# Optimization experiments

Measured on AMD Instinct MI355X. Metric: run time of the kernel, lower is better.

Reference implementation:

```python
import jax, jax.numpy as jnp
import numpy as np

POOL = 7
IMG = 1024.0
NUM_CLASSES = 2
R = 1000


def crop_and_resize(feat, boxes, pool):
    # feat: [C,H,W]; boxes: [N,4] normalized (y1,x1,y2,x2); returns [N,C,pool,pool]
    C, H, W = feat.shape
    y1, x1, y2, x2 = boxes[:, 0], boxes[:, 1], boxes[:, 2], boxes[:, 3]
    t = jnp.arange(pool, dtype=feat.dtype) / (pool - 1)
    ys = (y1[:, None] + (y2 - y1)[:, None] * t[None, :]) * (H - 1)  # [N,P]
    xs = (x1[:, None] + (x2 - x1)[:, None] * t[None, :]) * (W - 1)  # [N,P]
    vy = (ys >= 0) & (ys <= H - 1)
    vx = (xs >= 0) & (xs <= W - 1)
    yf = jnp.floor(ys)
    xf = jnp.floor(xs)
    wy = (ys - yf)[None, :, :, None]  # [1,N,P,1]
    wx = (xs - xf)[None, :, None, :]  # [1,N,1,P]
    y0 = jnp.clip(yf, 0, H - 1).astype(jnp.int32)
    y1i = jnp.clip(yf + 1, 0, H - 1).astype(jnp.int32)
    x0 = jnp.clip(xf, 0, W - 1).astype(jnp.int32)
    x1i = jnp.clip(xf + 1, 0, W - 1).astype(jnp.int32)

    def g(yi, xi):  # gather -> [C,N,P,P]
        return feat[:, yi[:, :, None], xi[:, None, :]]

    val = (g(y0, x0) * (1 - wy) * (1 - wx)
           + g(y0, x1i) * (1 - wy) * wx
           + g(y1i, x0) * wy * (1 - wx)
           + g(y1i, x1i) * wy * wx)
    mask = (vy[:, :, None] & vx[:, None, :])[None]  # extrapolation value 0
    return jnp.where(mask, val, 0.0).transpose(1, 0, 2, 3)


def roi_align(feats, rois_flat):
    # rois_flat: [N,4] in pixel coords (x1,y1,x2,y2)
    x1, y1, x2, y2 = rois_flat[:, 0], rois_flat[:, 1], rois_flat[:, 2], rois_flat[:, 3]
    lvl = jnp.log2(jnp.sqrt((y2 - y1) * (x2 - x1)) / 224.0)
    lvl = jnp.clip(jnp.round(lvl) + 4, 2, 5)
    boxes = rois_flat[:, jnp.array([1, 0, 3, 2])] / IMG  # (y1,x1,y2,x2) normalized
    crops = jnp.stack([crop_and_resize(f[0], boxes, POOL) for f in feats])  # [4,N,C,P,P]
    sel = (lvl[None, :] == jnp.arange(2, 6, dtype=lvl.dtype)[:, None])       # [4,N]
    return jnp.sum(jnp.where(sel[:, :, None, None, None], crops, 0.0), axis=0)  # [N,C,P,P]


def setup_inputs() -> dict:
    key = jax.random.key(0)
    ks = jax.random.split(key, 24)
    feat2 = jax.random.normal(ks[0], (1, 256, 256, 256), jnp.float32)
    feat3 = jax.random.normal(ks[1], (1, 256, 128, 128), jnp.float32)
    feat4 = jax.random.normal(ks[2], (1, 256, 64, 64), jnp.float32)
    feat5 = jax.random.normal(ks[3], (1, 256, 32, 32), jnp.float32)
    x1 = jax.random.uniform(ks[4], (1, R), minval=0.0, maxval=900.0)
    y1 = jax.random.uniform(ks[5], (1, R), minval=0.0, maxval=900.0)
    w = jax.random.uniform(ks[6], (1, R), minval=16.0, maxval=400.0)
    h = jax.random.uniform(ks[7], (1, R), minval=16.0, maxval=400.0)
    rois = jnp.stack([x1, y1, jnp.minimum(x1 + w, 1023.0), jnp.minimum(y1 + h, 1023.0)], axis=-1)
    s = 0.02
    params = dict(
        conv_w=s * jax.random.normal(ks[8], (1024, 256, POOL, POOL), jnp.float32),
        conv_b=jnp.zeros((1024,), jnp.float32),
        bn_gamma=jnp.ones((1024,), jnp.float32),
        bn_beta=jnp.zeros((1024,), jnp.float32),
        bn_mean=jnp.zeros((1024,), jnp.float32),
        bn_var=jnp.ones((1024,), jnp.float32),
        fc1_w=s * jax.random.normal(ks[9], (1024, 1024), jnp.float32),
        fc1_b=jnp.zeros((1024,), jnp.float32),
        fc2_w=s * jax.random.normal(ks[10], (1024, 1024), jnp.float32),
        fc2_b=jnp.zeros((1024,), jnp.float32),
        cls_w=s * jax.random.normal(ks[11], (NUM_CLASSES, 1024), jnp.float32),
        cls_b=jnp.zeros((NUM_CLASSES,), jnp.float32),
        bbox_w=s * jax.random.normal(ks[12], (NUM_CLASSES * 4, 1024), jnp.float32),
        bbox_b=jnp.zeros((NUM_CLASSES * 4,), jnp.float32),
    )
    return dict(feat2=feat2, feat3=feat3, feat4=feat4, feat5=feat5, rois=rois, **params)


def reference(feat2, feat3, feat4, feat5, rois, conv_w, conv_b, bn_gamma, bn_beta,
              bn_mean, bn_var, fc1_w, fc1_b, fc2_w, fc2_b, cls_w, cls_b, bbox_w, bbox_b):
    roi_number = rois.shape[1]
    pooled = roi_align([feat2, feat3, feat4, feat5], rois.reshape(-1, 4))  # [N,256,7,7]
    # conv1 (7x7 valid on 7x7 input -> 1x1 spatial) + BN (inference stats, eps=1e-3)
    y = jnp.einsum('nchw,ochw->no', pooled, conv_w) + conv_b
    y = (y - bn_mean) / jnp.sqrt(bn_var + 1e-3) * bn_gamma + bn_beta
    h = jax.nn.relu(y @ fc1_w.T + fc1_b)
    h = jax.nn.relu(h @ fc2_w.T + fc2_b)
    logits = h @ cls_w.T + cls_b
    probs = jax.nn.softmax(logits, axis=-1)
    bbox = h @ bbox_w.T + bbox_b
    return (logits.reshape(1, roi_number, NUM_CLASSES),
            probs.reshape(1, roi_number, NUM_CLASSES),
            bbox.reshape(1, roi_number, NUM_CLASSES, 4))
```

## Files before the change

### kernel.cpp

```cpp
#include <hip/hip_runtime.h>
#include <cstdint>
#include <cstddef>

typedef __attribute__((ext_vector_type(8))) short bf16x8;
typedef __attribute__((ext_vector_type(4))) float f32x4;

#define POOLK 12544

#define TOFF2 0
#define TOFF3 16777216
#define TOFF4 20971520
#define TOFF5 22020096

__device__ __forceinline__ void gld16(const void* g, void* l) {
    __builtin_amdgcn_global_load_lds(
        (const __attribute__((address_space(1))) void*)g,
        (__attribute__((address_space(3))) void*)l, 16, 0, 0);
}
__device__ __forceinline__ unsigned short f32_to_bf16(float f) {
    union { float f; unsigned u; } x; x.f = f;
    return (unsigned short)((x.u + 0x7FFFu + ((x.u >> 16) & 1u)) >> 16);
}
__device__ __forceinline__ float bf16_to_f32(unsigned short s) {
    return __uint_as_float(((unsigned)s) << 16);
}

__global__ __launch_bounds__(256) void feat_tr_kernel(
    const float* __restrict__ f2, const float* __restrict__ f3,
    const float* __restrict__ f4, const float* __restrict__ f5,
    unsigned short* __restrict__ T)
{
    __shared__ __align__(16) unsigned short sh[128 * 256];
    int b = blockIdx.x;
    const float* src; unsigned short* dst; int P;
    if (b < 512)      { src = f2; dst = T + TOFF2; P = 65536; }
    else if (b < 640) { src = f3; dst = T + TOFF3; P = 16384; b -= 512; }
    else if (b < 672) { src = f4; dst = T + TOFF4; P = 4096;  b -= 640; }
    else              { src = f5; dst = T + TOFF5; P = 1024;  b -= 672; }
    const int p0 = b * 128;
    const int t = threadIdx.x;
    const int lane5 = t & 31;
    const int x4 = lane5 * 4;
    const int fx = (lane5 & 7) << 3;

#pragma unroll
    for (int it = 0; it < 8; ++it) {
        float4 v[4];
        int cs[4];
#pragma unroll
        for (int u = 0; u < 4; ++u) {
            cs[u] = it * 32 + u * 8 + (t >> 5);
            v[u] = *(const float4*)(src + (size_t)cs[u] * P + p0 + x4);
        }
#pragma unroll
        for (int u = 0; u < 4; ++u) {
            const int cp = cs[u] ^ fx;
            float vv[4] = {v[u].x, v[u].y, v[u].z, v[u].w};
#pragma unroll
            for (int i = 0; i < 4; ++i)
                sh[(x4 + i) * 256 + cp] = f32_to_bf16(vv[i]);
        }
    }
    __syncthreads();

    const int c0 = lane5 * 8;
#pragma unroll
    for (int oz = 0; oz < 16; ++oz) {
        const int pp = oz * 8 + (t >> 5);
        const int cr = c0 ^ (((pp >> 2) & 7) << 3);
        const bf16x8 vv = *(const bf16x8*)&sh[pp * 256 + cr];
        *(bf16x8*)(dst + (size_t)(p0 + pp) * 256 + c0) = vv;
    }
}

__global__ __launch_bounds__(256) void gather_prep_kernel(
    const unsigned short* __restrict__ T, const float* __restrict__ rois,
    unsigned short* __restrict__ pooled, int nroi,
    const float* __restrict__ conv_w, unsigned short* __restrict__ convw_bf,
    const float* __restrict__ fc1_w, unsigned short* __restrict__ fc1w_bf,
    const float* __restrict__ fc2_w, unsigned short* __restrict__ fc2w_bf)
{
    const int t = threadIdx.x;
    int b = blockIdx.x;

    if (b >= 2048) {
        b -= 2048;
        if (b < 1024) {
            __shared__ __align__(16) unsigned short shw[POOLK];
            const float* srow = conv_w + (size_t)b * POOLK;
            for (int k4 = t; k4 < 3136; k4 += 256) {
                const float4 v = *(const float4*)(srow + k4 * 4);
                ushort4 o4;
                o4.x = f32_to_bf16(v.x); o4.y = f32_to_bf16(v.y);
                o4.z = f32_to_bf16(v.z); o4.w = f32_to_bf16(v.w);
                *(ushort4*)(&shw[k4 * 4]) = o4;
            }
            __syncthreads();
            unsigned short* drow = convw_bf + (size_t)b * POOLK;
            for (int e = t; e < 1568; e += 256) {
                const int p = e * 8;
                const int ij = p >> 8, c0 = p & 255;
                bf16x8 o8;
#pragma unroll
                for (int c = 0; c < 8; ++c) o8[c] = (short)shw[(c0 + c) * 49 + ij];
                *(bf16x8*)(drow + p) = o8;
            }
        } else {
            b -= 1024;
            const float* src = (b < 256) ? fc1_w : fc2_w;
            unsigned short* dst = (b < 256) ? fc1w_bf : fc2w_bf;
            const int base = (b & 255) * 4096 + t * 16;
#pragma unroll
            for (int u = 0; u < 4; ++u) {
                const float4 v = *(const float4*)(src + base + u * 4);
                ushort4 o4;
                o4.x = f32_to_bf16(v.x); o4.y = f32_to_bf16(v.y);
                o4.z = f32_to_bf16(v.z); o4.w = f32_to_bf16(v.w);
                *(ushort4*)(dst + base + u * 4) = o4;
            }
        }
        return;
    }

    const int n = b >> 1;
    const int half = b & 1;
    unsigned short* orow = pooled + (size_t)n * POOLK;
    if (n >= nroi) {
        const bf16x8 z = {};
        const int base = half * 6272;
        for (int k = base + t * 8; k < base + 6272; k += 2048) *(bf16x8*)(orow + k) = z;
        return;
    }
    __shared__ int sy0[7], sy1[7], sx0[7], sx1[7];
    __shared__ float swy[7], swx[7], svy[7], svx[7];

    const float rx1 = rois[n*4+0], ry1 = rois[n*4+1];
    const float rx2 = rois[n*4+2], ry2 = rois[n*4+3];
    int lvl = (int)rintf(log2f(sqrtf((ry2-ry1)*(rx2-rx1)) * (1.0f/224.0f))) + 4;
    lvl = lvl < 2 ? 2 : (lvl > 5 ? 5 : lvl);
    const int W = 256 >> (lvl - 2);
    const float Hm1 = (float)(W - 1);
    const unsigned short* Tl = T + (lvl == 2 ? TOFF2 : (lvl == 3 ? TOFF3 : (lvl == 4 ? TOFF4 : TOFF5)));

    if (t < 7) {
        const float tt = (float)t / 6.0f;
        const float by1 = ry1*(1.0f/1024.0f), by2 = ry2*(1.0f/1024.0f);
        const float bx1 = rx1*(1.0f/1024.0f), bx2 = rx2*(1.0f/1024.0f);
        const float ys = (by1 + (by2 - by1) * tt) * Hm1;
        const float xs = (bx1 + (bx2 - bx1) * tt) * Hm1;
        const float yf = floorf(ys), xf = floorf(xs);
        swy[t] = ys - yf;  swx[t] = xs - xf;
        sy0[t] = (int)fminf(fmaxf(yf,        0.0f), Hm1);
        sy1[t] = (int)fminf(fmaxf(yf + 1.0f, 0.0f), Hm1);
        sx0[t] = (int)fminf(fmaxf(xf,        0.0f), Hm1);
        sx1[t] = (int)fminf(fmaxf(xf + 1.0f, 0.0f), Hm1);
        svy[t] = (ys >= 0.0f && ys <= Hm1) ? 1.0f : 0.0f;
        svx[t] = (xs >= 0.0f && xs <= Hm1) ? 1.0f : 0.0f;
    }
    __syncthreads();

    const int g    = t >> 5;
    const int c0   = (t & 31) * 8;
    const int pbeg = half * 25;
    const int pend = pbeg + 25 - half;
#pragma unroll
    for (int it = 0; it < 4; ++it) {
        const int pos = pbeg + it * 8 + g;
        if (pos >= pend) break;
        const int i = pos / 7, j = pos % 7;
        const int y0 = sy0[i], y1 = sy1[i], x0 = sx0[j], x1 = sx1[j];
        const float wy = swy[i], wx = swx[j];
        const float scale = svy[i] * svx[j];
        const bf16x8 v00 = *(const bf16x8*)(Tl + ((size_t)(y0*W + x0))*256 + c0);
        const bf16x8 v01 = *(const bf16x8*)(Tl + ((size_t)(y0*W + x1))*256 + c0);
        const bf16x8 v10 = *(const bf16x8*)(Tl + ((size_t)(y1*W + x0))*256 + c0);
        const bf16x8 v11 = *(const bf16x8*)(Tl + ((size_t)(y1*W + x1))*256 + c0);
        bf16x8 o;
#pragma unroll
        for (int jj = 0; jj < 8; ++jj) {
            const float f00 = bf16_to_f32((unsigned short)v00[jj]);
            const float f01 = bf16_to_f32((unsigned short)v01[jj]);
            const float f10 = bf16_to_f32((unsigned short)v10[jj]);
            const float f11 = bf16_to_f32((unsigned short)v11[jj]);
            const float top = f00 + (f01 - f00) * wx;
            const float bot = f10 + (f11 - f10) * wx;
            o[jj] = (short)f32_to_bf16((top + (bot - top) * wy) * scale);
        }
        *(bf16x8*)(orow + pos * 256 + c0) = o;
    }
}

__global__ __launch_bounds__(256) void roi_direct_kernel(
    const float* __restrict__ feat2, const float* __restrict__ feat3,
    const float* __restrict__ feat4, const float* __restrict__ feat5,
    const float* __restrict__ rois, unsigned short* __restrict__ pooled, int nroi)
{
    const int n = blockIdx.x;
    const int tid = threadIdx.x;
    unsigned short* orow = pooled + (size_t)n * POOLK;
    if (n >= nroi) {
        const bf16x8 z = {};
        for (int k = tid * 8; k < POOLK; k += 2048) *(bf16x8*)(orow + k) = z;
        return;
    }
    __shared__ int sy0[7], sy1[7], sx0[7], sx1[7];
    __shared__ float swy[7], swx[7], svy[7], svx[7];
    const float rx1 = rois[n*4+0], ry1 = rois[n*4+1];
    const float rx2 = rois[n*4+2], ry2 = rois[n*4+3];
    int lvl = (int)rintf(log2f(sqrtf((ry2-ry1)*(rx2-rx1)) * (1.0f/224.0f))) + 4;
    lvl = lvl < 2 ? 2 : (lvl > 5 ? 5 : lvl);
    const int H = 256 >> (lvl - 2);
    const float Hm1 = (float)(H - 1);
    const float* feat = lvl==2 ? feat2 : (lvl==3 ? feat3 : (lvl==4 ? feat4 : feat5));
    if (tid < 7) {
        const float t = (float)tid / 6.0f;
        const float by1 = ry1*(1.0f/1024.0f), by2 = ry2*(1.0f/1024.0f);
        const float bx1 = rx1*(1.0f/1024.0f), bx2 = rx2*(1.0f/1024.0f);
        const float ys = (by1 + (by2-by1)*t) * Hm1;
        const float xs = (bx1 + (bx2-bx1)*t) * Hm1;
        const float yf = floorf(ys), xf = floorf(xs);
        swy[tid] = ys - yf;  swx[tid] = xs - xf;
        sy0[tid] = (int)fminf(fmaxf(yf,      0.0f), Hm1);
        sy1[tid] = (int)fminf(fmaxf(yf+1.0f, 0.0f), Hm1);
        sx0[tid] = (int)fminf(fmaxf(xf,      0.0f), Hm1);
        sx1[tid] = (int)fminf(fmaxf(xf+1.0f, 0.0f), Hm1);
        svy[tid] = (ys >= 0.0f && ys <= Hm1) ? 1.0f : 0.0f;
        svx[tid] = (xs >= 0.0f && xs <= Hm1) ? 1.0f : 0.0f;
    }
    __syncthreads();
    const int HW = H * H;
    for (int e = tid; e < POOLK; e += 256) {
        const int c = e / 49, ij = e % 49, i = ij / 7, j = ij % 7;
        const float* p = feat + c * HW;
        const int y0 = sy0[i], y1 = sy1[i], x0 = sx0[j], x1 = sx1[j];
        const float wy = swy[i], wx = swx[j];
        const float v00 = p[y0*H + x0], v01 = p[y0*H + x1];
        const float v10 = p[y1*H + x0], v11 = p[y1*H + x1];
        float v = v00*(1.0f-wy)*(1.0f-wx) + v01*(1.0f-wy)*wx
                + v10*wy*(1.0f-wx)        + v11*wy*wx;
        v *= svy[i] * svx[j];
        orow[ij*256 + c] = f32_to_bf16(v);
    }
}

__global__ __launch_bounds__(256) void wprep_kernel(
    const float* __restrict__ conv_w, unsigned short* __restrict__ convw_bf,
    const float* __restrict__ fc1_w, unsigned short* __restrict__ fc1w_bf,
    const float* __restrict__ fc2_w, unsigned short* __restrict__ fc2w_bf)
{
    const int t = threadIdx.x;
    int b = blockIdx.x;
    if (b < 1024) {
        __shared__ __align__(16) unsigned short shw[POOLK];
        const float* srow = conv_w + (size_t)b * POOLK;
        for (int k4 = t; k4 < 3136; k4 += 256) {
            const float4 v = *(const float4*)(srow + k4 * 4);
            ushort4 o4;
            o4.x = f32_to_bf16(v.x); o4.y = f32_to_bf16(v.y);
            o4.z = f32_to_bf16(v.z); o4.w = f32_to_bf16(v.w);
            *(ushort4*)(&shw[k4 * 4]) = o4;
        }
        __syncthreads();
        unsigned short* drow = convw_bf + (size_t)b * POOLK;
        for (int e = t; e < 1568; e += 256) {
            const int p = e * 8;
            const int ij = p >> 8, c0 = p & 255;
            bf16x8 o8;
#pragma unroll
            for (int c = 0; c < 8; ++c) o8[c] = (short)shw[(c0 + c) * 49 + ij];
            *(bf16x8*)(drow + p) = o8;
        }
        return;
    }
    b -= 1024;
    const float* src = (b < 256) ? fc1_w : fc2_w;
    unsigned short* dst = (b < 256) ? fc1w_bf : fc2w_bf;
    const int base = (b & 255) * 4096 + t * 16;
#pragma unroll
    for (int u = 0; u < 4; ++u) {
        const float4 v = *(const float4*)(src + base + u * 4);
        ushort4 o4;
        o4.x = f32_to_bf16(v.x); o4.y = f32_to_bf16(v.y);
        o4.z = f32_to_bf16(v.z); o4.w = f32_to_bf16(v.w);
        *(ushort4*)(dst + base + u * 4) = o4;
    }
}

__global__ __launch_bounds__(256, 2) void gemm_bt(
    const unsigned short* __restrict__ A, const unsigned short* __restrict__ B,
    float* __restrict__ Cpart, int K, int Kper, int nz)
{
    __shared__ __align__(16) unsigned short At[2][128*64];
    __shared__ __align__(16) unsigned short Bt[2][128*64];
    const int tid  = threadIdx.x;
    const int lane = tid & 63;
    const int bid  = blockIdx.x;
    const int z  = bid % nz;
    const int iq = bid / nz;
    const int bx = iq & 7, by = iq >> 3;
    const int wm = (tid >> 6) >> 1, wn = (tid >> 6) & 1;
    const size_t k0 = (size_t)z * Kper;

    const int r1 = tid >> 3;
    const int q  = tid & 7;
    const int csw = (q ^ (r1 & 7)) * 8;
    const unsigned short* Ag = A + ((size_t)(by * 128 + r1)) * K + k0 + csw;
    const unsigned short* Bg = B + ((size_t)(bx * 128 + r1)) * K + k0 + csw;
    const int nit = (Kper + 63) >> 6;

#pragma unroll
    for (int p = 0; p < 4; ++p) {
        gld16(Ag + (size_t)(32 * p) * K, &At[0][p * 2048 + tid * 8]);
        gld16(Bg + (size_t)(32 * p) * K, &Bt[0][p * 2048 + tid * 8]);
    }

    f32x4 acc[4][4] = {};
    const int fr = lane & 15;
    const int fq = lane >> 4;
    const int sA = fr & 7;

    int buf = 0;
    for (int it = 0; it < nit; ++it) {
        const int k = it << 6;
        if (it + 1 < nit) {
            const size_t ko = (size_t)(k + 64);
#pragma unroll
            for (int p = 0; p < 4; ++p) {
                gld16(Ag + (size_t)(32 * p) * K + ko, &At[buf ^ 1][p * 2048 + tid * 8]);
                gld16(Bg + (size_t)(32 * p) * K + ko, &Bt[buf ^ 1][p * 2048 + tid * 8]);
            }
            asm volatile("s_waitcnt vmcnt(8)" ::: "memory");
        } else {
            asm volatile("s_waitcnt vmcnt(0)" ::: "memory");
        }
        __builtin_amdgcn_sched_barrier(0);
        __builtin_amdgcn_s_barrier();
        __builtin_amdgcn_sched_barrier(0);

        bf16x8 a[4][2], b[4][2];
#pragma unroll
        for (int mi = 0; mi < 4; ++mi) {
            const int row = wm * 64 + mi * 16 + fr;
#pragma unroll
            for (int kk = 0; kk < 2; ++kk)
                a[mi][kk] = *(const bf16x8*)&At[buf][row * 64 + ((kk * 4 + fq) ^ sA) * 8];
        }
#pragma unroll
        for (int ni = 0; ni < 4; ++ni) {
            const int row = wn * 64 + ni * 16 + fr;
#pragma unroll
            for (int kk = 0; kk < 2; ++kk)
                b[ni][kk] = *(const bf16x8*)&Bt[buf][row * 64 + ((kk * 4 + fq) ^ sA) * 8];
        }
        __builtin_amdgcn_s_setprio(1);
#pragma unroll
        for (int mi = 0; mi < 4; ++mi)
#pragma unroll
            for (int ni = 0; ni < 4; ++ni)
                acc[mi][ni] = __builtin_amdgcn_mfma_f32_16x16x32_bf16(
                    a[mi][0], b[ni][0], acc[mi][ni], 0, 0, 0);
        if (k + 32 < Kper) {
#pragma unroll
            for (int mi = 0; mi < 4; ++mi)
#pragma unroll
                for (int ni = 0; ni < 4; ++ni)
                    acc[mi][ni] = __builtin_amdgcn_mfma_f32_16x16x32_bf16(
                        a[mi][1], b[ni][1], acc[mi][ni], 0, 0, 0);
        }
        __builtin_amdgcn_s_setprio(0);
        __builtin_amdgcn_sched_barrier(0);
        __builtin_amdgcn_s_barrier();
        __builtin_amdgcn_sched_barrier(0);
        buf ^= 1;
    }

    float* Cp = Cpart + (size_t)z * (1024 * 1024);
    const int row0 = by * 128 + wm * 64;
    const int col0 = bx * 128 + wn * 64;
#pragma unroll
    for (int mi = 0; mi < 4; ++mi)
#pragma unroll
        for (int ni = 0; ni < 4; ++ni)
#pragma unroll
            for (int r = 0; r < 4; ++r)
                Cp[(size_t)(row0 + mi*16 + fq*4 + r) * 1024 + col0 + ni*16 + fr]
                    = acc[mi][ni][r];
}

__global__ void reduce_bn_kernel(const float* __restrict__ part,
    const float* __restrict__ bias, const float* __restrict__ gamma,
    const float* __restrict__ beta, const float* __restrict__ mean,
    const float* __restrict__ var, unsigned short* __restrict__ out, int nz)
{
    const int i4 = (blockIdx.x * 256 + threadIdx.x) * 4;
    const int n = i4 & 1023;
    float4 v = make_float4(0.f, 0.f, 0.f, 0.f);
    for (int zz = 0; zz < nz; ++zz) {
        const float4 p = *(const float4*)(part + (size_t)zz * 1048576 + i4);
        v.x += p.x; v.y += p.y; v.z += p.z; v.w += p.w;
    }
    const float4 bi = *(const float4*)(bias + n);
    const float4 ga = *(const float4*)(gamma + n);
    const float4 be = *(const float4*)(beta + n);
    const float4 me = *(const float4*)(mean + n);
    const float4 va = *(const float4*)(var + n);
    ushort4 o;
    o.x = f32_to_bf16((v.x + bi.x - me.x) * __frsqrt_rn(va.x + 0.001f) * ga.x + be.x);
    o.y = f32_to_bf16((v.y + bi.y - me.y) * __frsqrt_rn(va.y + 0.001f) * ga.y + be.y);
    o.z = f32_to_bf16((v.z + bi.z - me.z) * __frsqrt_rn(va.z + 0.001f) * ga.z + be.z);
    o.w = f32_to_bf16((v.w + bi.w - me.w) * __frsqrt_rn(va.w + 0.001f) * ga.w + be.w);
    *(ushort4*)(out + i4) = o;
}

__global__ __launch_bounds__(256) void gemm64_fused(
    const unsigned short* __restrict__ A, const unsigned short* __restrict__ B,
    const float* __restrict__ bias, unsigned short* __restrict__ out, int relu)
{
    __shared__ __align__(16) unsigned short At[2][64*64];
    __shared__ __align__(16) unsigned short Bt[2][64*64];
    const int tid = threadIdx.x, lane = tid & 63;
    const int w = tid >> 6, wm = w >> 1, wn = w & 1;
    const int r1 = tid >> 3;
    const int q  = tid & 7;
    const int csw = (q ^ (r1 & 7)) * 8;
    const unsigned short* Ag = A + (size_t)(blockIdx.y*64 + r1) * 1024 + csw;
    const unsigned short* Bg = B + (size_t)(blockIdx.x*64 + r1) * 1024 + csw;
    const int fr = lane & 15, fq = lane >> 4;
    const int sA = fr & 7;

#pragma unroll
    for (int p = 0; p < 2; ++p) {
        gld16(Ag + (size_t)(32 * p) * 1024, &At[0][p * 2048 + tid * 8]);
        gld16(Bg + (size_t)(32 * p) * 1024, &Bt[0][p * 2048 + tid * 8]);
    }

    f32x4 acc[2][2] = {};
    int buf = 0;
    for (int it = 0; it < 16; ++it) {
        if (it + 1 < 16) {
            const int ko = (it + 1) * 64;
#pragma unroll
            for (int p = 0; p < 2; ++p) {
                gld16(Ag + (size_t)(32 * p) * 1024 + ko, &At[buf ^ 1][p * 2048 + tid * 8]);
                gld16(Bg + (size_t)(32 * p) * 1024 + ko, &Bt[buf ^ 1][p * 2048 + tid * 8]);
            }
            asm volatile("s_waitcnt vmcnt(4)" ::: "memory");
        } else {
            asm volatile("s_waitcnt vmcnt(0)" ::: "memory");
        }
        __builtin_amdgcn_sched_barrier(0);
        __builtin_amdgcn_s_barrier();
        __builtin_amdgcn_sched_barrier(0);

        bf16x8 a[2][2], b[2][2];
#pragma unroll
        for (int mi = 0; mi < 2; ++mi) {
            const int row = wm * 32 + mi * 16 + fr;
#pragma unroll
            for (int kk = 0; kk < 2; ++kk)
                a[mi][kk] = *(const bf16x8*)&At[buf][row * 64 + ((kk * 4 + fq) ^ sA) * 8];
        }
#pragma unroll
        for (int ni = 0; ni < 2; ++ni) {
            const int row = wn * 32 + ni * 16 + fr;
#pragma unroll
            for (int kk = 0; kk < 2; ++kk)
                b[ni][kk] = *(const bf16x8*)&Bt[buf][row * 64 + ((kk * 4 + fq) ^ sA) * 8];
        }
        __builtin_amdgcn_s_setprio(1);
#pragma unroll
        for (int kk = 0; kk < 2; ++kk)
#pragma unroll
            for (int mi = 0; mi < 2; ++mi)
#pragma unroll
                for (int ni = 0; ni < 2; ++ni)
                    acc[mi][ni] = __builtin_amdgcn_mfma_f32_16x16x32_bf16(
                        a[mi][kk], b[ni][kk], acc[mi][ni], 0, 0, 0);
        __builtin_amdgcn_s_setprio(0);
        __builtin_amdgcn_sched_barrier(0);
        __builtin_amdgcn_s_barrier();
        __builtin_amdgcn_sched_barrier(0);
        buf ^= 1;
    }
    const int row0 = blockIdx.y*64 + wm*32;
    const int col0 = blockIdx.x*64 + wn*32;
#pragma unroll
    for (int mi = 0; mi < 2; ++mi)
#pragma unroll
        for (int ni = 0; ni < 2; ++ni)
#pragma unroll
            for (int r = 0; r < 4; ++r) {
                const int row = row0 + mi*16 + fq*4 + r;
                const int col = col0 + ni*16 + fr;
                float v = acc[mi][ni][r] + bias[col];
                if (relu) v = fmaxf(v, 0.0f);
                out[(size_t)row * 1024 + col] = f32_to_bf16(v);
            }
}

__global__ __launch_bounds__(256) void head_kernel(
    const unsigned short* __restrict__ h2,
    const float* __restrict__ cls_w, const float* __restrict__ cls_b,
    const float* __restrict__ bbox_w, const float* __restrict__ bbox_b,
    float* __restrict__ out)
{
    const int roi = blockIdx.x * 4 + (threadIdx.x >> 6);
    const int lane = threadIdx.x & 63;
    const unsigned short* hrow = h2 + (size_t)roi * 1024;
    float hv[16];
#pragma unroll
    for (int j = 0; j < 16; ++j)
        hv[j] = bf16_to_f32(hrow[lane*16 + j]);
    float r[10];
#pragma unroll
    for (int o = 0; o < 10; ++o) {
        const float* w = (o < 2) ? (cls_w + o*1024) : (bbox_w + (size_t)(o-2)*1024);
        float s = 0.f;
#pragma unroll
        for (int j = 0; j < 16; ++j) s += hv[j] * w[lane*16 + j];
#pragma unroll
        for (int off = 32; off > 0; off >>= 1) s += __shfl_xor(s, off);
        r[o] = s;
    }
    if (lane == 0) {
        const float l0 = r[0] + cls_b[0], l1 = r[1] + cls_b[1];
        out[roi*2+0] = l0; out[roi*2+1] = l1;
        const float m = fmaxf(l0, l1);
        const float e0 = expf(l0 - m), e1 = expf(l1 - m);
        const float inv = 1.0f / (e0 + e1);
        out[2000 + roi*2 + 0] = e0 * inv;
        out[2000 + roi*2 + 1] = e1 * inv;
#pragma unroll
        for (int qq = 0; qq < 8; ++qq) out[4000 + roi*8 + qq] = r[2+qq] + bbox_b[qq];
    }
}

extern "C" void kernel_launch(void* const* d_in, const int* in_sizes, int n_in,
                              void* d_out, int out_size, void* d_ws, size_t ws_size,
                              hipStream_t stream)
{
    const float* feat2   = (const float*)d_in[0];
    const float* feat3   = (const float*)d_in[1];
    const float* feat4   = (const float*)d_in[2];
    const float* feat5   = (const float*)d_in[3];
    const float* rois    = (const float*)d_in[4];
    const float* conv_w  = (const float*)d_in[5];
    const float* conv_b  = (const float*)d_in[6];
    const float* bn_gamma= (const float*)d_in[7];
    const float* bn_beta = (const float*)d_in[8];
    const float* bn_mean = (const float*)d_in[9];
    const float* bn_var  = (const float*)d_in[10];
    const float* fc1_w   = (const float*)d_in[11];
    const float* fc1_b   = (const float*)d_in[12];
    const float* fc2_w   = (const float*)d_in[13];
    const float* fc2_b   = (const float*)d_in[14];
    const float* cls_w   = (const float*)d_in[15];
    const float* cls_b   = (const float*)d_in[16];
    const float* bbox_w  = (const float*)d_in[17];
    const float* bbox_b  = (const float*)d_in[18];
    float* out = (float*)d_out;
    const int nroi = in_sizes[4] / 4;

    const size_t fixedBytes = (size_t)25690112 + 25690112 + 5 * (size_t)2097152;
    const size_t needA = fixedBytes + (size_t)44564480;
    const int tier = (ws_size >= needA) ? 1 : 2;
    const size_t regionA = tier == 1 ? (size_t)44564480 : (size_t)16777216;
    const int nzc  = tier == 1 ? 8 : 4;
    const int Kper = tier == 1 ? 1568 : 3136;

    char* ws = (char*)d_ws;
    size_t off = 0;
    auto alloc = [&](size_t bytes) {
        void* p = ws + off; off += (bytes + 255) & ~(size_t)255; return p;
    };
    char* rA = (char*)alloc(regionA);
    unsigned short* T    = (unsigned short*)rA;
    float*          part = (float*)rA;
    unsigned short* pooled   = (unsigned short*)alloc((size_t)1024 * POOLK * 2);
    unsigned short* convw_bf = (unsigned short*)alloc((size_t)1024 * POOLK * 2);
    unsigned short* fc1w_bf  = (unsigned short*)alloc((size_t)1048576 * 2);
    unsigned short* fc2w_bf  = (unsigned short*)alloc((size_t)1048576 * 2);
    unsigned short* ybf      = (unsigned short*)alloc((size_t)1048576 * 2);
    unsigned short* h1bf     = (unsigned short*)alloc((size_t)1048576 * 2);
    unsigned short* h2bf     = (unsigned short*)alloc((size_t)1048576 * 2);

    if (tier == 1) {
        hipLaunchKernelGGL(feat_tr_kernel, dim3(680), dim3(256), 0, stream,
                           feat2, feat3, feat4, feat5, T);
        hipLaunchKernelGGL(gather_prep_kernel, dim3(3584), dim3(256), 0, stream,
                           T, rois, pooled, nroi,
                           conv_w, convw_bf, fc1_w, fc1w_bf, fc2_w, fc2w_bf);
    } else {
        hipLaunchKernelGGL(wprep_kernel, dim3(1536), dim3(256), 0, stream,
                           conv_w, convw_bf, fc1_w, fc1w_bf, fc2_w, fc2w_bf);
        hipLaunchKernelGGL(roi_direct_kernel, dim3(1024), dim3(256), 0, stream,
                           feat2, feat3, feat4, feat5, rois, pooled, nroi);
    }

    hipLaunchKernelGGL(gemm_bt, dim3(64 * nzc), dim3(256), 0, stream,
                       pooled, convw_bf, part, POOLK, Kper, nzc);
    hipLaunchKernelGGL(reduce_bn_kernel, dim3(1024), dim3(256), 0, stream,
                       part, conv_b, bn_gamma, bn_beta, bn_mean, bn_var, ybf, nzc);

    hipLaunchKernelGGL(gemm64_fused, dim3(16, 16), dim3(256), 0, stream,
                       ybf, fc1w_bf, fc1_b, h1bf, 1);
    hipLaunchKernelGGL(gemm64_fused, dim3(16, 16), dim3(256), 0, stream,
                       h1bf, fc2w_bf, fc2_b, h2bf, 1);

    hipLaunchKernelGGL(head_kernel, dim3(250), dim3(256), 0, stream,
                       h2bf, cls_w, cls_b, bbox_w, bbox_b, out);
}
```

Baseline: 125.6 us.

## Store split-K partials in bf16 and interleave weight-prep blocks with gather blocks

The split-K conv GEMM now writes its partial sums as bf16 instead of fp32, and the reduce+BN kernel reads bf16 partials. This halves partial-sum write and read traffic at the cost of extra rounding error accumulated across the K splits. Separately, the fused gather/weight-prep kernel remaps block indices so that each group of 7 blocks mixes 4 gather blocks, 2 conv-weight blocks and 1 fc-weight block. The aim is to overlap the bandwidth-bound weight conversion with the gather work instead of running it as a tail.

```diff
diff --git a/kernel.cpp b/kernel.cpp
--- a/kernel.cpp
+++ b/kernel.cpp
@@ -81,13 +81,13 @@
     const float* __restrict__ fc2_w, unsigned short* __restrict__ fc2w_bf)
 {
     const int t = threadIdx.x;
-    int b = blockIdx.x;
-
-    if (b >= 2048) {
-        b -= 2048;
-        if (b < 1024) {
+    const int grp = blockIdx.x / 7, rem = blockIdx.x % 7;
+
+    if (rem >= 4) {
+        if (rem < 6) {
+            const int o = grp * 2 + (rem - 4);
             __shared__ __align__(16) unsigned short shw[POOLK];
-            const float* srow = conv_w + (size_t)b * POOLK;
+            const float* srow = conv_w + (size_t)o * POOLK;
             for (int k4 = t; k4 < 3136; k4 += 256) {
                 const float4 v = *(const float4*)(srow + k4 * 4);
                 ushort4 o4;
@@ -96,7 +96,7 @@
                 *(ushort4*)(&shw[k4 * 4]) = o4;
             }
             __syncthreads();
-            unsigned short* drow = convw_bf + (size_t)b * POOLK;
+            unsigned short* drow = convw_bf + (size_t)o * POOLK;
             for (int e = t; e < 1568; e += 256) {
                 const int p = e * 8;
                 const int ij = p >> 8, c0 = p & 255;
@@ -106,10 +106,10 @@
                 *(bf16x8*)(drow + p) = o8;
             }
         } else {
-            b -= 1024;
-            const float* src = (b < 256) ? fc1_w : fc2_w;
-            unsigned short* dst = (b < 256) ? fc1w_bf : fc2w_bf;
-            const int base = (b & 255) * 4096 + t * 16;
+            const int bb = grp;
+            const float* src = (bb < 256) ? fc1_w : fc2_w;
+            unsigned short* dst = (bb < 256) ? fc1w_bf : fc2w_bf;
+            const int base = (bb & 255) * 4096 + t * 16;
 #pragma unroll
             for (int u = 0; u < 4; ++u) {
                 const float4 v = *(const float4*)(src + base + u * 4);
@@ -122,8 +122,9 @@
         return;
     }
 
-    const int n = b >> 1;
-    const int half = b & 1;
+    const int gb = grp * 4 + rem;
+    const int n = gb >> 1;
+    const int half = gb & 1;
     unsigned short* orow = pooled + (size_t)n * POOLK;
     if (n >= nroi) {
         const bf16x8 z = {};
@@ -288,7 +289,7 @@
 
 __global__ __launch_bounds__(256, 2) void gemm_bt(
     const unsigned short* __restrict__ A, const unsigned short* __restrict__ B,
-    float* __restrict__ Cpart, int K, int Kper, int nz)
+    unsigned short* __restrict__ Cpart, int K, int Kper, int nz)
 {
     __shared__ __align__(16) unsigned short At[2][128*64];
     __shared__ __align__(16) unsigned short Bt[2][128*64];
@@ -374,7 +375,7 @@
         buf ^= 1;
     }
 
-    float* Cp = Cpart + (size_t)z * (1024 * 1024);
+    unsigned short* Cp = Cpart + (size_t)z * (1024 * 1024);
     const int row0 = by * 128 + wm * 64;
     const int col0 = bx * 128 + wn * 64;
 #pragma unroll
@@ -384,10 +385,10 @@
 #pragma unroll
             for (int r = 0; r < 4; ++r)
                 Cp[(size_t)(row0 + mi*16 + fq*4 + r) * 1024 + col0 + ni*16 + fr]
-                    = acc[mi][ni][r];
-}
-
-__global__ void reduce_bn_kernel(const float* __restrict__ part,
+                    = f32_to_bf16(acc[mi][ni][r]);
+}
+
+__global__ void reduce_bn_kernel(const unsigned short* __restrict__ part,
     const float* __restrict__ bias, const float* __restrict__ gamma,
     const float* __restrict__ beta, const float* __restrict__ mean,
     const float* __restrict__ var, unsigned short* __restrict__ out, int nz)
@@ -396,8 +397,9 @@
     const int n = i4 & 1023;
     float4 v = make_float4(0.f, 0.f, 0.f, 0.f);
     for (int zz = 0; zz < nz; ++zz) {
-        const float4 p = *(const float4*)(part + (size_t)zz * 1048576 + i4);
-        v.x += p.x; v.y += p.y; v.z += p.z; v.w += p.w;
+        const ushort4 p = *(const ushort4*)(part + (size_t)zz * 1048576 + i4);
+        v.x += bf16_to_f32(p.x); v.y += bf16_to_f32(p.y);
+        v.z += bf16_to_f32(p.z); v.w += bf16_to_f32(p.w);
     }
     const float4 bi = *(const float4*)(bias + n);
     const float4 ga = *(const float4*)(gamma + n);
@@ -575,7 +577,7 @@
     };
     char* rA = (char*)alloc(regionA);
     unsigned short* T    = (unsigned short*)rA;
-    float*          part = (float*)rA;
+    unsigned short* part = (unsigned short*)rA;
     unsigned short* pooled   = (unsigned short*)alloc((size_t)1024 * POOLK * 2);
     unsigned short* convw_bf = (unsigned short*)alloc((size_t)1024 * POOLK * 2);
     unsigned short* fc1w_bf  = (unsigned short*)alloc((size_t)1048576 * 2);
```

New measurement: 125.3 us. About the same (-0.2%).
